# Performance work log

Hardware: AMD Instinct MI355X
Metric: run time of the kernel (lower is better)

The kernel has to match this reference:

```python
import jax, jax.numpy as jnp
import numpy as np

B, L, DW, DP = 128, 512, 256, 64
NF = 512          # num_filters == types == nr (forced by U.view / maxpool in source)
D = DW + 2 * DP   # 384
DWIN = 3 * D      # windowed feature width


def setup_inputs() -> dict:
    key = jax.random.key(0)
    ks = jax.random.split(key, 10)
    return {
        "x": jax.random.normal(ks[0], (B, L, DW), jnp.float32),
        "e1": jax.random.normal(ks[1], (B, DW), jnp.float32),
        "e2": jax.random.normal(ks[2], (B, DW), jnp.float32),
        "posVec": jax.random.normal(ks[3], (B, L, 2 * DP), jnp.float32),
        "We1": jax.random.normal(ks[4], (DW, DW), jnp.float32),
        "We2": jax.random.normal(ks[5], (DW, DW), jnp.float32),
        "U": jax.random.normal(ks[6], (NF, NF), jnp.float32),
        "conv_w": jax.random.normal(ks[7], (NF, DWIN), jnp.float32) * 0.02,
        "conv_b": jnp.zeros((NF,), jnp.float32),
        "rel_w": jax.random.normal(ks[8], (NF, NF), jnp.float32) * 0.02,  # y_embedding.weight (nr, num_filters)
    }


def reference(x, e1, e2, posVec, We1, We2, U, conv_w, conv_b, rel_w):
    # ---- input attention ----
    x_concat = jnp.concatenate([x, posVec], axis=-1)            # (B, L, D)
    px = jnp.pad(x_concat, ((0, 0), (1, 1), (0, 0)))            # pad seq by k=1
    w_concat = jnp.concatenate(
        [px[:, 0:L], px[:, 1:L + 1], px[:, 2:L + 2]], axis=-1)  # (B, L, 3D)
    A1 = jnp.einsum('bld,de,be->bl', x, We1, e1)                # (B, L)
    A2 = jnp.einsum('bld,de,be->bl', x, We2, e2)
    alpha = 0.5 * (jax.nn.softmax(A1, axis=1) + jax.nn.softmax(A2, axis=1))
    R = w_concat * alpha[:, :, None]                            # (B, L, 3D)
    # ---- convolution (kernel spans full window -> per-position linear) ----
    conv = jnp.tanh(jnp.einsum('bld,fd->bfl', R, conv_w) + conv_b[None, :, None])  # (B, F, L)
    # ---- attentive pooling ----
    G = jnp.einsum('bfl,ft,rt->blr', conv, U, rel_w)            # (B, L, nr)
    AP = jax.nn.softmax(G, axis=1)                              # softmax over seq positions
    wo = jnp.einsum('bfl,blr->bfr', conv, AP)                   # (B, F, nr)
    wo = jnp.max(wo, axis=2)                                    # MaxPool2d((1, types)) -> (B, F)
    wo = jax.nn.relu(wo)
    return wo, rel_w
```

## Files before the change

kernel.cpp:

```cpp
#include <hip/hip_runtime.h>
#include <hip/hip_bf16.h>

#define BB 128
#define LL 512
#define DW 256
#define DP 64
#define NF 512
#define DD 384
#define DWIN 1152
#define RR 512
#define LP 514

typedef __attribute__((ext_vector_type(8))) short short8;
typedef __attribute__((ext_vector_type(4))) short short4v;
typedef __attribute__((ext_vector_type(2))) short short2v;
typedef __attribute__((ext_vector_type(8))) _Float16 half8;
typedef __attribute__((ext_vector_type(4))) float f32x4;
typedef __attribute__((ext_vector_type(2))) float f32x2;

typedef __attribute__((address_space(1))) const void* gas_t;
typedef __attribute__((address_space(3))) void* las_t;

__device__ __forceinline__ void stage16(const void* g, void* l) {
    __builtin_amdgcn_global_load_lds((gas_t)g, (las_t)l, 16, 0, 0);
}

__device__ inline short f2h(float v) {
    _Float16 h = (_Float16)v;
    return *reinterpret_cast<short*>(&h);
}
__device__ inline int xcd_swz(int bid, int nwg) {
    return (bid & 7) * (nwg >> 3) + (bid >> 3);
}

__global__ void k_ve(const float* __restrict__ We1, const float* __restrict__ We2,
                     const float* __restrict__ e1, const float* __restrict__ e2,
                     float* __restrict__ v1, float* __restrict__ v2) {
    int b = blockIdx.x;
    int d = threadIdx.x;
    __shared__ float s1[DW], s2[DW];
    s1[d] = e1[b * DW + d];
    s2[d] = e2[b * DW + d];
    __syncthreads();
    float a1 = 0.f, a2 = 0.f;
    for (int e = 0; e < DW; ++e) {
        a1 += We1[d * DW + e] * s1[e];
        a2 += We2[d * DW + e] * s2[e];
    }
    v1[b * DW + d] = a1;
    v2[b * DW + d] = a2;
}

__global__ __launch_bounds__(256) void k_pack_logits(
    const float* __restrict__ x, const float* __restrict__ pv,
    const float* __restrict__ v1, const float* __restrict__ v2,
    short* __restrict__ pxp, float* __restrict__ A1, float* __restrict__ A2) {
    int gr = blockIdx.x * 4 + (threadIdx.x >> 6);
    int lane = threadIdx.x & 63;
    int b = gr / LP;
    int rr = gr - b * LP;
    short* dst = pxp + (size_t)gr * DD;
    if (rr == 0 || rr == LP - 1) {
        *(short4v*)(dst + lane * 4) = (short4v){0, 0, 0, 0};
        *(short2v*)(dst + 256 + lane * 2) = (short2v){0, 0};
        return;
    }
    int l = rr - 1;
    f32x4 xv = *(const f32x4*)(x + ((size_t)b * LL + l) * DW + lane * 4);
    f32x2 pvv = *(const f32x2*)(pv + ((size_t)b * LL + l) * (2 * DP) + lane * 2);
    f32x4 w1 = *(const f32x4*)(v1 + b * DW + lane * 4);
    f32x4 w2 = *(const f32x4*)(v2 + b * DW + lane * 4);
    float p1 = xv[0] * w1[0] + xv[1] * w1[1] + xv[2] * w1[2] + xv[3] * w1[3];
    float p2 = xv[0] * w2[0] + xv[1] * w2[1] + xv[2] * w2[2] + xv[3] * w2[3];
    for (int off = 32; off; off >>= 1) {
        p1 += __shfl_down(p1, off);
        p2 += __shfl_down(p2, off);
    }
    short4v ox;
#pragma unroll
    for (int j = 0; j < 4; ++j) ox[j] = f2h(xv[j]);
    *(short4v*)(dst + lane * 4) = ox;
    short2v op;
    op[0] = f2h(pvv[0]);
    op[1] = f2h(pvv[1]);
    *(short2v*)(dst + 256 + lane * 2) = op;
    if (lane == 0) { A1[b * LL + l] = p1; A2[b * LL + l] = p2; }
}

__global__ void k_alpha(const float* __restrict__ A1, const float* __restrict__ A2,
                        float* __restrict__ alpha) {
    int b = blockIdx.x;
    int l = threadIdx.x;
    __shared__ float s[LL];
    float a1 = A1[b * LL + l], a2 = A2[b * LL + l];

    s[l] = a1; __syncthreads();
    for (int st = 256; st; st >>= 1) { if (l < st) s[l] = fmaxf(s[l], s[l + st]); __syncthreads(); }
    float m1 = s[0]; __syncthreads();
    float e1x = expf(a1 - m1);
    s[l] = e1x; __syncthreads();
    for (int st = 256; st; st >>= 1) { if (l < st) s[l] += s[l + st]; __syncthreads(); }
    float d1 = s[0]; __syncthreads();

    s[l] = a2; __syncthreads();
    for (int st = 256; st; st >>= 1) { if (l < st) s[l] = fmaxf(s[l], s[l + st]); __syncthreads(); }
    float m2 = s[0]; __syncthreads();
    float e2x = expf(a2 - m2);
    s[l] = e2x; __syncthreads();
    for (int st = 256; st; st >>= 1) { if (l < st) s[l] += s[l + st]; __syncthreads(); }
    float d2 = s[0];

    alpha[b * LL + l] = 0.5f * (e1x / d1 + e2x / d2);
}

__global__ __launch_bounds__(256) void k_pack_w(const float* __restrict__ cw,
                                                short* __restrict__ cwb) {
    int idx = blockIdx.x * 256 + threadIdx.x;
    const float* src = cw + (size_t)idx * 8;
    f32x4 u0 = *(const f32x4*)(src);
    f32x4 u1 = *(const f32x4*)(src + 4);
    short8 v;
#pragma unroll
    for (int jj = 0; jj < 4; ++jj) { v[jj] = f2h(u0[jj]); v[jj + 4] = f2h(u1[jj]); }
    *(short8*)(cwb + (size_t)idx * 8) = v;
}

__global__ void k_w2t(const float* __restrict__ U, const float* __restrict__ relw,
                      short* __restrict__ Qf) {
    __shared__ float As[16][65], Bs[16][65];
    int r0 = blockIdx.y * 64, f0 = blockIdx.x * 64;
    int tid = threadIdx.x, ty = tid >> 4, tx = tid & 15;
    float acc[4][4] = {};
    for (int k0 = 0; k0 < NF; k0 += 16) {
        for (int i = 0; i < 4; ++i) {
            int lin = tid + 256 * i;
            int kk = lin & 15, mm = lin >> 4;
            As[kk][mm] = relw[(r0 + mm) * NF + k0 + kk];
            Bs[kk][mm] = U[(f0 + mm) * NF + k0 + kk];
        }
        __syncthreads();
        for (int kk = 0; kk < 16; ++kk) {
            float av[4], bv[4];
            for (int i = 0; i < 4; ++i) av[i] = As[kk][ty * 4 + i];
            for (int j = 0; j < 4; ++j) bv[j] = Bs[kk][tx * 4 + j];
            for (int i = 0; i < 4; ++i)
                for (int j = 0; j < 4; ++j) acc[i][j] += av[i] * bv[j];
        }
        __syncthreads();
    }
    for (int i = 0; i < 4; ++i)
        for (int j = 0; j < 4; ++j)
            Qf[(size_t)(r0 + ty * 4 + i) * NF + f0 + tx * 4 + j] = f2h(acc[i][j]);
}

__global__ __launch_bounds__(256) void k_conv_mfma(
    const short* __restrict__ pxp, const short* __restrict__ cwb,
    const float* __restrict__ conv_b, const float* __restrict__ alpha,
    short* __restrict__ conv_lf, short* __restrict__ conv_fl) {
    int wg = xcd_swz(blockIdx.x, 2048);
    int b = wg >> 4;
    int l0 = ((wg >> 2) & 3) * 128;
    int f0 = (wg & 3) * 128;
    int tid = threadIdx.x;
    int lane = tid & 63, w = tid >> 6;
    int wm = w >> 1, wn = w & 1;
    int lr = lane & 15, lg = lane >> 4;

    __shared__ __align__(16) char smem[34816];
    short (*T)[136] = (short(*)[136])smem;

    f32x4 acc[4][4];
    for (int i = 0; i < 4; ++i)
        for (int j = 0; j < 4; ++j) acc[i][j] = (f32x4){0.f, 0.f, 0.f, 0.f};

    int rowA = lane >> 2;
    int sw = (lane & 3) ^ ((rowA >> 1) & 3);
    const short* gA = pxp + ((size_t)b * LP + l0 + w * 32 + rowA) * DD + sw * 8;
    const short* gB = cwb + (size_t)(f0 + w * 32 + rowA) * DWIN + sw * 8;
    int rsw = (lg ^ ((lr >> 1) & 3)) * 8;
    int rA = wm * 64, rB = wn * 64;

    {
        char* nbuf = smem;
        stage16(gA, nbuf + w * 2048);
        stage16(gA + 16 * DD, nbuf + w * 2048 + 1024);
        stage16(gB, nbuf + 8192 + w * 2048);
        stage16(gB + (size_t)16 * DWIN, nbuf + 8192 + w * 2048 + 1024);
    }

    for (int t = 0; t < 36; ++t) {
        char* cbuf = smem + (t & 1) * 16384;
        if (t + 1 < 36) {
            char* nbuf = smem + ((t + 1) & 1) * 16384;
            int k0 = (t + 1) * 32;
            stage16(gA + k0, nbuf + w * 2048);
            stage16(gA + 16 * DD + k0, nbuf + w * 2048 + 1024);
            stage16(gB + k0, nbuf + 8192 + w * 2048);
            stage16(gB + (size_t)16 * DWIN + k0, nbuf + 8192 + w * 2048 + 1024);
            asm volatile("s_waitcnt vmcnt(4)" ::: "memory");
        } else {
            asm volatile("s_waitcnt vmcnt(0)" ::: "memory");
        }
        __builtin_amdgcn_s_barrier();
        __builtin_amdgcn_sched_barrier(0);
        const short (*Ac)[32] = (const short(*)[32])cbuf;
        const short (*Bc)[32] = (const short(*)[32])(cbuf + 8192);
        half8 af[4], bf[4];
#pragma unroll
        for (int mi = 0; mi < 4; ++mi)
            af[mi] = *(const half8*)(&Ac[rA + mi * 16 + lr][rsw]);
#pragma unroll
        for (int ni = 0; ni < 4; ++ni)
            bf[ni] = *(const half8*)(&Bc[rB + ni * 16 + lr][rsw]);
#pragma unroll
        for (int mi = 0; mi < 4; ++mi)
#pragma unroll
            for (int ni = 0; ni < 4; ++ni)
                acc[mi][ni] = __builtin_amdgcn_mfma_f32_16x16x32_f16(
                    af[mi], bf[ni], acc[mi][ni], 0, 0, 0);
        __builtin_amdgcn_sched_barrier(0);
        __builtin_amdgcn_s_barrier();
        __builtin_amdgcn_sched_barrier(0);
    }

    int lbase = l0 + wm * 64, fbase = f0 + wn * 64;
#pragma unroll
    for (int mi = 0; mi < 4; ++mi) {
        f32x4 av = *(const f32x4*)(alpha + (size_t)b * LL + lbase + mi * 16 + lg * 4);
        int lrow = lbase + mi * 16 + lg * 4;
#pragma unroll
        for (int ni = 0; ni < 4; ++ni) {
            int f = fbase + ni * 16 + lr;
            float bias = conv_b[f];
            short4v o;
#pragma unroll
            for (int r = 0; r < 4; ++r) {
                float val = tanhf(av[r] * acc[mi][ni][r] + bias);
                short sv = f2h(val);
                o[r] = sv;
                conv_lf[((size_t)b * LL + lrow + r) * NF + f] = sv;
            }
            *(short4v*)(&T[wn * 64 + ni * 16 + lr][wm * 64 + mi * 16 + lg * 4]) = o;
        }
    }
    __syncthreads();
#pragma unroll
    for (int i = 0; i < 8; ++i) {
        int lin = tid + 256 * i;
        int frow = lin >> 4;
        int q = lin & 15;
        short8 v = *(const short8*)(&T[frow][q * 8]);
        *(short8*)(conv_fl + ((size_t)b * NF + f0 + frow) * LL + l0 + q * 8) = v;
    }
}

__global__ __launch_bounds__(512) void k_g_mfma(
    const short* __restrict__ Qf,
    const short* __restrict__ convlf, _Float16* __restrict__ Gp) {
    const float LOG2E = 1.4426950408889634f;
    int wg = xcd_swz(blockIdx.x, 512);
    int b = wg >> 2;
    int r0 = (wg & 3) * 128;
    int tid = threadIdx.x, lane = tid & 63, w = tid >> 6;
    int wm = w >> 2, wn = w & 3;
    int lr = lane & 15, lg = lane >> 4;

    __shared__ __align__(16) char smem[81920];
    short* Ab = (short*)smem;
    short* Bb = (short*)(smem + 16384);
    float (*rowred)[4] = (float(*)[4])smem;

    f32x4 acc[4][8];
#pragma unroll
    for (int i = 0; i < 4; ++i)
#pragma unroll
        for (int j = 0; j < 8; ++j) acc[i][j] = (f32x4){0.f, 0.f, 0.f, 0.f};

    int trow = tid >> 3;
    int sw = (tid & 7) ^ (trow & 7);
    const short* gA = Qf + (size_t)(r0 + trow) * NF + sw * 8;
    const short* gB = convlf + (size_t)b * LL * NF + (size_t)trow * NF + sw * 8;
    short* lAd = Ab + w * 512;
    short* lBd = Bb + w * 512;
    int p7 = lr & 7;

    for (int kb = 0; kb < 8; ++kb) {
        int k0 = kb * 64;
#pragma unroll
        for (int c = 0; c < 2; ++c)
            stage16(gA + (size_t)(64 * c) * NF + k0, lAd + c * 4096);
#pragma unroll
        for (int c = 0; c < 8; ++c)
            stage16(gB + (size_t)(64 * c) * NF + k0, lBd + c * 4096);
        __syncthreads();
#pragma unroll
        for (int kk = 0; kk < 2; ++kk) {
            int cs = (kk << 2) + lg;
            half8 af[4], bf[8];
#pragma unroll
            for (int mi = 0; mi < 4; ++mi)
                af[mi] = *(const half8*)(Ab + (wm * 64 + mi * 16 + lr) * 64 + ((cs ^ p7) * 8));
#pragma unroll
            for (int ni = 0; ni < 8; ++ni)
                bf[ni] = *(const half8*)(Bb + (wn * 128 + ni * 16 + lr) * 64 + ((cs ^ p7) * 8));
#pragma unroll
            for (int mi = 0; mi < 4; ++mi)
#pragma unroll
                for (int ni = 0; ni < 8; ++ni)
                    acc[mi][ni] = __builtin_amdgcn_mfma_f32_16x16x32_f16(
                        af[mi], bf[ni], acc[mi][ni], 0, 0, 0);
        }
        __syncthreads();
    }

    float mrow[4][4];
#pragma unroll
    for (int mi = 0; mi < 4; ++mi)
#pragma unroll
        for (int rr = 0; rr < 4; ++rr) {
            float m = acc[mi][0][rr];
#pragma unroll
            for (int ni = 1; ni < 8; ++ni) m = fmaxf(m, acc[mi][ni][rr]);
            m = fmaxf(m, __shfl_xor(m, 1));
            m = fmaxf(m, __shfl_xor(m, 2));
            m = fmaxf(m, __shfl_xor(m, 4));
            m = fmaxf(m, __shfl_xor(m, 8));
            mrow[mi][rr] = m;
        }
    if (lr == 0) {
#pragma unroll
        for (int mi = 0; mi < 4; ++mi)
#pragma unroll
            for (int rr = 0; rr < 4; ++rr)
                rowred[wm * 64 + mi * 16 + lg * 4 + rr][wn] = mrow[mi][rr];
    }
    __syncthreads();
#pragma unroll
    for (int mi = 0; mi < 4; ++mi)
#pragma unroll
        for (int rr = 0; rr < 4; ++rr) {
            f32x4 rv = *(const f32x4*)rowred[wm * 64 + mi * 16 + lg * 4 + rr];
            mrow[mi][rr] = fmaxf(fmaxf(rv[0], rv[1]), fmaxf(rv[2], rv[3]));
        }
    __syncthreads();
    float srow[4][4];
#pragma unroll
    for (int mi = 0; mi < 4; ++mi)
#pragma unroll
        for (int rr = 0; rr < 4; ++rr) {
            float s = 0.f;
            float m = mrow[mi][rr];
#pragma unroll
            for (int ni = 0; ni < 8; ++ni) {
                float pp = exp2f((acc[mi][ni][rr] - m) * LOG2E);
                acc[mi][ni][rr] = pp;
                s += pp;
            }
            s += __shfl_xor(s, 1);
            s += __shfl_xor(s, 2);
            s += __shfl_xor(s, 4);
            s += __shfl_xor(s, 8);
            srow[mi][rr] = s;
        }
    if (lr == 0) {
#pragma unroll
        for (int mi = 0; mi < 4; ++mi)
#pragma unroll
            for (int rr = 0; rr < 4; ++rr)
                rowred[wm * 64 + mi * 16 + lg * 4 + rr][wn] = srow[mi][rr];
    }
    __syncthreads();
#pragma unroll
    for (int mi = 0; mi < 4; ++mi)
#pragma unroll
        for (int rr = 0; rr < 4; ++rr) {
            f32x4 rv = *(const f32x4*)rowred[wm * 64 + mi * 16 + lg * 4 + rr];
            srow[mi][rr] = 1.f / (rv[0] + rv[1] + rv[2] + rv[3]);
        }

#pragma unroll
    for (int mi = 0; mi < 4; ++mi)
#pragma unroll
        for (int ni = 0; ni < 8; ++ni)
#pragma unroll
            for (int rr = 0; rr < 4; ++rr) {
                int r = r0 + wm * 64 + mi * 16 + lg * 4 + rr;
                int l = wn * 128 + ni * 16 + lr;
                Gp[((size_t)b * RR + r) * LL + l] = (_Float16)(acc[mi][ni][rr] * srow[mi][rr]);
            }
}

__global__ __launch_bounds__(256) void k_wo_mfma(
    const short* __restrict__ convfl, const short* __restrict__ P,
    float* __restrict__ out) {
    int wg = xcd_swz(blockIdx.x, 2048);
    int b = wg >> 4;
    int f0 = ((wg >> 2) & 3) * 128;
    int r0 = (wg & 3) * 128;
    int tid = threadIdx.x, lane = tid & 63, w = tid >> 6;
    int wm = w >> 1, wn = w & 1;
    int lr = lane & 15, lg = lane >> 4;

    __shared__ __align__(16) char smem[65536];

    f32x4 acc[4][4];
    for (int i = 0; i < 4; ++i)
        for (int j = 0; j < 4; ++j) acc[i][j] = (f32x4){0.f, 0.f, 0.f, 0.f};

    int rowA = lane >> 3;
    int sw = (lane & 7) ^ rowA;
    const short* gA = convfl + (size_t)b * NF * LL + (size_t)(f0 + w * 32 + rowA) * LL + sw * 8;
    const short* gB = P + (size_t)b * RR * LL + (size_t)(r0 + w * 32 + rowA) * LL + sw * 8;
    int rA = wm * 64, rB = wn * 64;
    int p7 = lr & 7;

    {
        char* nbuf = smem;
#pragma unroll
        for (int c = 0; c < 4; ++c) {
            stage16(gA + (size_t)(8 * c) * LL, nbuf + w * 4096 + c * 1024);
            stage16(gB + (size_t)(8 * c) * LL, nbuf + 16384 + w * 4096 + c * 1024);
        }
    }

    for (int t = 0; t < 8; ++t) {
        char* cbuf = smem + (t & 1) * 32768;
        if (t + 1 < 8) {
            char* nbuf = smem + ((t + 1) & 1) * 32768;
            int k0 = (t + 1) * 64;
#pragma unroll
            for (int c = 0; c < 4; ++c) {
                stage16(gA + (size_t)(8 * c) * LL + k0, nbuf + w * 4096 + c * 1024);
                stage16(gB + (size_t)(8 * c) * LL + k0, nbuf + 16384 + w * 4096 + c * 1024);
            }
            asm volatile("s_waitcnt vmcnt(8)" ::: "memory");
        } else {
            asm volatile("s_waitcnt vmcnt(0)" ::: "memory");
        }
        __builtin_amdgcn_s_barrier();
        __builtin_amdgcn_sched_barrier(0);
        const short (*Ac)[64] = (const short(*)[64])cbuf;
        const short (*Bc)[64] = (const short(*)[64])(cbuf + 16384);
#pragma unroll
        for (int kk = 0; kk < 2; ++kk) {
            half8 af[4], bf[4];
            int cs = ((kk << 2) + lg);
#pragma unroll
            for (int mi = 0; mi < 4; ++mi)
                af[mi] = *(const half8*)(&Ac[rA + mi * 16 + lr][(cs ^ p7) * 8]);
#pragma unroll
            for (int ni = 0; ni < 4; ++ni)
                bf[ni] = *(const half8*)(&Bc[rB + ni * 16 + lr][(cs ^ p7) * 8]);
#pragma unroll
            for (int mi = 0; mi < 4; ++mi)
#pragma unroll
                for (int ni = 0; ni < 4; ++ni)
                    acc[mi][ni] = __builtin_amdgcn_mfma_f32_16x16x32_f16(
                        af[mi], bf[ni], acc[mi][ni], 0, 0, 0);
        }
        __builtin_amdgcn_sched_barrier(0);
        __builtin_amdgcn_s_barrier();
        __builtin_amdgcn_sched_barrier(0);
    }

    int fbase = f0 + wm * 64;
#pragma unroll
    for (int mi = 0; mi < 4; ++mi)
#pragma unroll
        for (int rr = 0; rr < 4; ++rr) {
            float m = acc[mi][0][rr];
#pragma unroll
            for (int ni = 1; ni < 4; ++ni) m = fmaxf(m, acc[mi][ni][rr]);
            m = fmaxf(m, __shfl_xor(m, 1));
            m = fmaxf(m, __shfl_xor(m, 2));
            m = fmaxf(m, __shfl_xor(m, 4));
            m = fmaxf(m, __shfl_xor(m, 8));
            if (lr == 0 && m > 0.f) {
                int f = fbase + mi * 16 + lg * 4 + rr;
                atomicMax((int*)&out[(size_t)b * NF + f], __float_as_int(m));
            }
        }
}

extern "C" void kernel_launch(void* const* d_in, const int* in_sizes, int n_in,
                              void* d_out, int out_size, void* d_ws, size_t ws_size,
                              hipStream_t stream) {
    const float* x      = (const float*)d_in[0];
    const float* e1     = (const float*)d_in[1];
    const float* e2     = (const float*)d_in[2];
    const float* posVec = (const float*)d_in[3];
    const float* We1    = (const float*)d_in[4];
    const float* We2    = (const float*)d_in[5];
    const float* U      = (const float*)d_in[6];
    const float* conv_w = (const float*)d_in[7];
    const float* conv_b = (const float*)d_in[8];
    const float* rel_w  = (const float*)d_in[9];
    float* out = (float*)d_out;

    char* p = (char*)d_ws;
    short* convlf = (short*)p;  p += (size_t)BB * LL * NF * 2;
    short* convfl = (short*)p;  p += (size_t)BB * NF * LL * 2;
    _Float16* Gp  = (_Float16*)p;  p += (size_t)BB * RR * LL * 2;
    short* pxp    = (short*)p;  p += (size_t)BB * LP * DD * 2;
    short* cwb    = (short*)p;  p += (size_t)NF * DWIN * 2;
    short* QfW    = (short*)p;  p += (size_t)RR * NF * 2;
    float* v1     = (float*)p;  p += (size_t)BB * DW * 4;
    float* v2     = (float*)p;  p += (size_t)BB * DW * 4;
    float* A1     = (float*)p;  p += (size_t)BB * LL * 4;
    float* A2     = (float*)p;  p += (size_t)BB * LL * 4;
    float* alpha  = (float*)p;  p += (size_t)BB * LL * 4;

    k_ve<<<BB, DW, 0, stream>>>(We1, We2, e1, e2, v1, v2);
    k_pack_logits<<<(BB * LP) / 4, 256, 0, stream>>>(x, posVec, v1, v2, pxp, A1, A2);
    k_alpha<<<BB, LL, 0, stream>>>(A1, A2, alpha);
    k_pack_w<<<(NF * DWIN / 8) / 256, 256, 0, stream>>>(conv_w, cwb);
    k_w2t<<<dim3(NF / 64, RR / 64), 256, 0, stream>>>(U, rel_w, QfW);
    k_conv_mfma<<<2048, 256, 0, stream>>>(pxp, cwb, conv_b, alpha, convlf, convfl);
    k_g_mfma<<<512, 512, 0, stream>>>(QfW, convlf, Gp);
    hipMemsetAsync(d_out, 0, (size_t)BB * NF * sizeof(float), stream);
    k_wo_mfma<<<2048, 256, 0, stream>>>(convfl, (const short*)Gp, out);
    hipMemcpyAsync(out + BB * NF, rel_w, (size_t)NF * RR * sizeof(float),
                   hipMemcpyDeviceToDevice, stream);
}
```

Before: 326.7 us.

## Enlarge conv GEMM tiles to 256x256 with 512 threads and 64-wide K steps

The convolution MFMA kernel now has each workgroup of 8 waves compute a 256x256 output tile instead of 128x128, stepping K by 64 with a 128KB double-buffered LDS stage. It uses a new XOR swizzle for both operand staging and the transpose buffer, and raises wave priority around the MFMA bursts. The goal is more operand reuse per byte loaded and fewer barriers per unit of compute. In exchange, LDS use allows only one workgroup per CU, and the 512-block grid leaves less room to hide latency.

```diff
diff --git a/kernel.cpp b/kernel.cpp
--- a/kernel.cpp
+++ b/kernel.cpp
@@ -153,84 +153,98 @@
             Qf[(size_t)(r0 + ty * 4 + i) * NF + f0 + tx * 4 + j] = f2h(acc[i][j]);
 }
 
-__global__ __launch_bounds__(256) void k_conv_mfma(
+__global__ __launch_bounds__(512, 2) void k_conv_mfma(
     const short* __restrict__ pxp, const short* __restrict__ cwb,
     const float* __restrict__ conv_b, const float* __restrict__ alpha,
     short* __restrict__ conv_lf, short* __restrict__ conv_fl) {
-    int wg = xcd_swz(blockIdx.x, 2048);
-    int b = wg >> 4;
-    int l0 = ((wg >> 2) & 3) * 128;
-    int f0 = (wg & 3) * 128;
+    int wg = xcd_swz(blockIdx.x, 512);
+    int b = wg >> 2;
+    int bl0 = ((wg >> 1) & 1) * 256;
+    int bf0 = (wg & 1) * 256;
     int tid = threadIdx.x;
     int lane = tid & 63, w = tid >> 6;
-    int wm = w >> 1, wn = w & 1;
+    int wm = w >> 2, wn = w & 3;
     int lr = lane & 15, lg = lane >> 4;
 
-    __shared__ __align__(16) char smem[34816];
-    short (*T)[136] = (short(*)[136])smem;
-
-    f32x4 acc[4][4];
-    for (int i = 0; i < 4; ++i)
+    __shared__ __align__(16) char smem[131072];
+
+    f32x4 acc[8][4];
+#pragma unroll
+    for (int i = 0; i < 8; ++i)
+#pragma unroll
         for (int j = 0; j < 4; ++j) acc[i][j] = (f32x4){0.f, 0.f, 0.f, 0.f};
 
-    int rowA = lane >> 2;
-    int sw = (lane & 3) ^ ((rowA >> 1) & 3);
-    const short* gA = pxp + ((size_t)b * LP + l0 + w * 32 + rowA) * DD + sw * 8;
-    const short* gB = cwb + (size_t)(f0 + w * 32 + rowA) * DWIN + sw * 8;
-    int rsw = (lg ^ ((lr >> 1) & 3)) * 8;
-    int rA = wm * 64, rB = wn * 64;
+    int srow = lane >> 3;
+    int sw = (lane & 7) ^ srow;
+    const short* gA = pxp + ((size_t)b * LP + bl0 + w * 8 + srow) * DD + sw * 8;
+    const short* gB = cwb + (size_t)(bf0 + w * 8 + srow) * DWIN + sw * 8;
+    int p7 = lr & 7;
 
     {
-        char* nbuf = smem;
-        stage16(gA, nbuf + w * 2048);
-        stage16(gA + 16 * DD, nbuf + w * 2048 + 1024);
-        stage16(gB, nbuf + 8192 + w * 2048);
-        stage16(gB + (size_t)16 * DWIN, nbuf + 8192 + w * 2048 + 1024);
-    }
-
-    for (int t = 0; t < 36; ++t) {
-        char* cbuf = smem + (t & 1) * 16384;
-        if (t + 1 < 36) {
-            char* nbuf = smem + ((t + 1) & 1) * 16384;
-            int k0 = (t + 1) * 32;
-            stage16(gA + k0, nbuf + w * 2048);
-            stage16(gA + 16 * DD + k0, nbuf + w * 2048 + 1024);
-            stage16(gB + k0, nbuf + 8192 + w * 2048);
-            stage16(gB + (size_t)16 * DWIN + k0, nbuf + 8192 + w * 2048 + 1024);
-            asm volatile("s_waitcnt vmcnt(4)" ::: "memory");
-        } else {
-            asm volatile("s_waitcnt vmcnt(0)" ::: "memory");
-        }
-        __builtin_amdgcn_s_barrier();
-        __builtin_amdgcn_sched_barrier(0);
-        const short (*Ac)[32] = (const short(*)[32])cbuf;
-        const short (*Bc)[32] = (const short(*)[32])(cbuf + 8192);
-        half8 af[4], bf[4];
-#pragma unroll
-        for (int mi = 0; mi < 4; ++mi)
-            af[mi] = *(const half8*)(&Ac[rA + mi * 16 + lr][rsw]);
+        char* nb = smem;
+#pragma unroll
+        for (int c = 0; c < 4; ++c) {
+            stage16(gA + (size_t)(64 * c) * DD, nb + (c * 64 + w * 8) * 128);
+            stage16(gB + (size_t)(64 * c) * DWIN, nb + 32768 + (c * 64 + w * 8) * 128);
+        }
+    }
+    __syncthreads();
+
+    for (int kt = 0; kt < 18; ++kt) {
+        const char* cb = smem + (kt & 1) * 65536;
+        if (kt + 1 < 18) {
+            char* nb = smem + ((kt + 1) & 1) * 65536;
+            int k0 = (kt + 1) * 64;
+#pragma unroll
+            for (int c = 0; c < 4; ++c) {
+                stage16(gA + (size_t)(64 * c) * DD + k0, nb + (c * 64 + w * 8) * 128);
+                stage16(gB + (size_t)(64 * c) * DWIN + k0, nb + 32768 + (c * 64 + w * 8) * 128);
+            }
+        }
+        half8 bf[4][2];
 #pragma unroll
         for (int ni = 0; ni < 4; ++ni)
-            bf[ni] = *(const half8*)(&Bc[rB + ni * 16 + lr][rsw]);
-#pragma unroll
-        for (int mi = 0; mi < 4; ++mi)
-#pragma unroll
-            for (int ni = 0; ni < 4; ++ni)
-                acc[mi][ni] = __builtin_amdgcn_mfma_f32_16x16x32_f16(
-                    af[mi], bf[ni], acc[mi][ni], 0, 0, 0);
-        __builtin_amdgcn_sched_barrier(0);
-        __builtin_amdgcn_s_barrier();
-        __builtin_amdgcn_sched_barrier(0);
-    }
-
-    int lbase = l0 + wm * 64, fbase = f0 + wn * 64;
-#pragma unroll
-    for (int mi = 0; mi < 4; ++mi) {
-        f32x4 av = *(const f32x4*)(alpha + (size_t)b * LL + lbase + mi * 16 + lg * 4);
-        int lrow = lbase + mi * 16 + lg * 4;
+#pragma unroll
+            for (int ks = 0; ks < 2; ++ks) {
+                int cs = ks * 4 + lg;
+                bf[ni][ks] = *(const half8*)(cb + 32768 +
+                    (wn * 64 + ni * 16 + lr) * 128 + ((cs ^ p7) * 16));
+            }
+#pragma unroll
+        for (int mh = 0; mh < 2; ++mh) {
+            half8 af[4][2];
+#pragma unroll
+            for (int mi = 0; mi < 4; ++mi)
+#pragma unroll
+                for (int ks = 0; ks < 2; ++ks) {
+                    int cs = ks * 4 + lg;
+                    af[mi][ks] = *(const half8*)(cb +
+                        (wm * 128 + mh * 64 + mi * 16 + lr) * 128 + ((cs ^ p7) * 16));
+                }
+            __builtin_amdgcn_s_setprio(1);
+#pragma unroll
+            for (int mi = 0; mi < 4; ++mi)
+#pragma unroll
+                for (int ni = 0; ni < 4; ++ni)
+#pragma unroll
+                    for (int ks = 0; ks < 2; ++ks)
+                        acc[mh * 4 + mi][ni] = __builtin_amdgcn_mfma_f32_16x16x32_f16(
+                            af[mi][ks], bf[ni][ks], acc[mh * 4 + mi][ni], 0, 0, 0);
+            __builtin_amdgcn_s_setprio(0);
+        }
+        __syncthreads();
+    }
+
+    char* T = smem;
+#pragma unroll
+    for (int mi = 0; mi < 8; ++mi) {
+        int lloc = wm * 128 + mi * 16 + lg * 4;
+        int l = bl0 + lloc;
+        f32x4 av = *(const f32x4*)(alpha + (size_t)b * LL + l);
 #pragma unroll
         for (int ni = 0; ni < 4; ++ni) {
-            int f = fbase + ni * 16 + lr;
+            int floc = wn * 64 + ni * 16 + lr;
+            int f = bf0 + floc;
             float bias = conv_b[f];
             short4v o;
 #pragma unroll
@@ -238,19 +252,20 @@
                 float val = tanhf(av[r] * acc[mi][ni][r] + bias);
                 short sv = f2h(val);
                 o[r] = sv;
-                conv_lf[((size_t)b * LL + lrow + r) * NF + f] = sv;
-            }
-            *(short4v*)(&T[wn * 64 + ni * 16 + lr][wm * 64 + mi * 16 + lg * 4]) = o;
+                conv_lf[((size_t)b * LL + l + r) * NF + f] = sv;
+            }
+            int c16 = lloc >> 3;
+            *(short4v*)(T + floc * 512 + ((c16 ^ (floc & 31)) << 4) + (lloc & 7) * 2) = o;
         }
     }
     __syncthreads();
 #pragma unroll
-    for (int i = 0; i < 8; ++i) {
-        int lin = tid + 256 * i;
-        int frow = lin >> 4;
-        int q = lin & 15;
-        short8 v = *(const short8*)(&T[frow][q * 8]);
-        *(short8*)(conv_fl + ((size_t)b * NF + f0 + frow) * LL + l0 + q * 8) = v;
+    for (int i = 0; i < 16; ++i) {
+        int lin = tid + 512 * i;
+        int frow = lin >> 5;
+        int c16 = lin & 31;
+        short8 v = *(const short8*)(T + frow * 512 + ((c16 ^ (frow & 31)) << 4));
+        *(short8*)(conv_fl + ((size_t)b * NF + bf0 + frow) * LL + bl0 + c16 * 8) = v;
     }
 }
 
@@ -515,7 +530,7 @@
     k_alpha<<<BB, LL, 0, stream>>>(A1, A2, alpha);
     k_pack_w<<<(NF * DWIN / 8) / 256, 256, 0, stream>>>(conv_w, cwb);
     k_w2t<<<dim3(NF / 64, RR / 64), 256, 0, stream>>>(U, rel_w, QfW);
-    k_conv_mfma<<<2048, 256, 0, stream>>>(pxp, cwb, conv_b, alpha, convlf, convfl);
+    k_conv_mfma<<<512, 512, 0, stream>>>(pxp, cwb, conv_b, alpha, convlf, convfl);
     k_g_mfma<<<512, 512, 0, stream>>>(QfW, convlf, Gp);
     hipMemsetAsync(d_out, 0, (size_t)BB * NF * sizeof(float), stream);
     k_wo_mfma<<<2048, 256, 0, stream>>>(convfl, (const short*)Gp, out);
```

Measured after the change: 315.5 us. 1.04x faster.
